# Performance work log

Measured on AMD Instinct MI355X. Metric: run time of the kernel, lower is better.

The kernel has to match this reference:

```python
import jax, jax.numpy as jnp
import numpy as np

B, C, IMG, P, G = 512, 3, 128, 16, 8
DIM, HEADS, DH, DEPTH, MLP, NCLS, K = 384, 6, 64, 12, 1536, 1000, 16
N = G * G + 1  # 65 tokens (cls + 8x8 patches)
INNER = HEADS * DH
PD = C * P * P  # patch_dim = 768


def _rel_pos_index(g):
    coords = np.stack(np.meshgrid(np.arange(g), np.arange(g), indexing='ij')).reshape(2, -1)
    rel = (coords[:, :, None] - coords[:, None, :]).transpose(1, 2, 0)
    rel[..., 0] += g - 1
    rel[..., 1] += g - 1
    rel[..., 0] *= 2 * g - 1
    return jnp.asarray(rel.sum(-1))  # [g*g, g*g] int

REL_IDX = _rel_pos_index(G)


def _ln(x, w, b, eps=1e-5):
    mu = jnp.mean(x, -1, keepdims=True)
    var = jnp.mean((x - mu) ** 2, -1, keepdims=True)
    return (x - mu) * jax.lax.rsqrt(var + eps) * w + b


def setup_inputs() -> dict:
    key = jax.random.key(0)
    ks = iter(jax.random.split(key, 48))
    nrm = lambda shape, s=0.02: jax.random.normal(next(ks), shape, jnp.float32) * s
    return {
        'img': jax.random.normal(next(ks), (B, C, IMG, IMG), jnp.float32),
        'pe_ln1_w': jnp.ones((PD,), jnp.float32), 'pe_ln1_b': jnp.zeros((PD,), jnp.float32),
        'pe_w': nrm((PD, DIM)), 'pe_b': jnp.zeros((DIM,), jnp.float32),
        'pe_ln2_w': jnp.ones((DIM,), jnp.float32), 'pe_ln2_b': jnp.zeros((DIM,), jnp.float32),
        'cls_token': nrm((1, DIM), 1.0), 'pos_emb': nrm((N, DIM), 1.0),
        'attn_ln_w': jnp.ones((DEPTH, DIM), jnp.float32), 'attn_ln_b': jnp.zeros((DEPTH, DIM), jnp.float32),
        'qkv_w': nrm((DEPTH, DIM, 3 * INNER)),
        'out_w': nrm((DEPTH, INNER, DIM)), 'out_b': jnp.zeros((DEPTH, DIM), jnp.float32),
        'bias_tables': nrm((DEPTH, (2 * G - 1) * (2 * G - 1))),
        'ff_ln_w': jnp.ones((DEPTH, DIM), jnp.float32), 'ff_ln_b': jnp.zeros((DEPTH, DIM), jnp.float32),
        'ff_w1': nrm((DEPTH, DIM, MLP)), 'ff_b1': jnp.zeros((DEPTH, MLP), jnp.float32),
        'ff_w2': nrm((DEPTH, MLP, DIM)), 'ff_b2': jnp.zeros((DEPTH, DIM), jnp.float32),
        'final_ln_w': jnp.ones((DIM,), jnp.float32), 'final_ln_b': jnp.zeros((DIM,), jnp.float32),
        'head_w': nrm((DIM, NCLS)), 'head_b': jnp.zeros((NCLS,), jnp.float32),
    }


def reference(img, pe_ln1_w, pe_ln1_b, pe_w, pe_b, pe_ln2_w, pe_ln2_b, cls_token, pos_emb,
              attn_ln_w, attn_ln_b, qkv_w, out_w, out_b, bias_tables,
              ff_ln_w, ff_ln_b, ff_w1, ff_b1, ff_w2, ff_b2,
              final_ln_w, final_ln_b, head_w, head_b):
    b = img.shape[0]
    gh = IMG // P
    # b c (h p1) (w p2) -> b (h w) (p1 p2 c)
    x = img.reshape(b, C, gh, P, gh, P).transpose(0, 2, 4, 3, 5, 1).reshape(b, gh * gh, P * P * C)
    x = _ln(x, pe_ln1_w, pe_ln1_b)
    x = _ln(x @ pe_w + pe_b, pe_ln2_w, pe_ln2_b)
    cls = jnp.broadcast_to(cls_token[None], (b, 1, DIM))
    x = jnp.concatenate([cls, x], axis=1) + pos_emb[:N]
    scale = DH ** -0.5
    neg = jnp.finfo(jnp.float32).min  # == -finfo.max, matching torch masked_fill
    for i in range(DEPTH):
        h = _ln(x, attn_ln_w[i], attn_ln_b[i])
        qkv = h @ qkv_w[i]  # [b, N, 3*INNER]
        q, k, v = jnp.split(qkv, 3, axis=-1)
        q, k, v = [t.reshape(b, N, HEADS, DH).transpose(0, 2, 1, 3) for t in (q, k, v)]
        dots = jnp.einsum('bhid,bhjd->bhij', q, k) * scale
        full_bias = jnp.zeros((N, N), jnp.float32).at[1:, 1:].set(bias_tables[i][REL_IDX])
        dots = dots + full_bias
        _, idx = jax.lax.top_k(dots, K)  # per-query top-k keys
        mask = jnp.put_along_axis(jnp.zeros(dots.shape, bool), idx, True, axis=-1, inplace=False)
        attn = jax.nn.softmax(jnp.where(mask, dots, neg), axis=-1)
        o = jnp.einsum('bhij,bhjd->bhid', attn, v).transpose(0, 2, 1, 3).reshape(b, N, INNER)
        x = o @ out_w[i] + out_b[i] + x
        h = _ln(x, ff_ln_w[i], ff_ln_b[i])
        h = jax.nn.gelu(h @ ff_w1[i] + ff_b1[i], approximate=False)
        x = h @ ff_w2[i] + ff_b2[i] + x
    x = _ln(x, final_ln_w, final_ln_b)
    return x[:, 0] @ head_w + head_b
```

## Files before the change

### kernel.cpp

```cpp
#include <hip/hip_runtime.h>
#include <cstdint>
#include <cstddef>


typedef __attribute__((ext_vector_type(8))) short bf16x8;
typedef __attribute__((ext_vector_type(4))) float f32x4;
typedef __attribute__((ext_vector_type(4))) unsigned short u16x4;

__device__ __forceinline__ unsigned short f2bf(float f) {
  unsigned u = __float_as_uint(f);
  u += 0x7FFF + ((u >> 16) & 1);
  return (unsigned short)(u >> 16);
}
__device__ __forceinline__ float bf2f(unsigned short h) {
  return __uint_as_float(((unsigned)h) << 16);
}
__device__ __forceinline__ float gelu_f(float v) {
  return 0.5f * v * (1.f + erff(v * 0.70710678118654752440f));
}

typedef const __attribute__((address_space(1))) unsigned int* gas1_t;
typedef __attribute__((address_space(3))) unsigned int* las3_t;
__device__ __forceinline__ void async16(const void* g, void* l) {
  __builtin_amdgcn_global_load_lds((gas1_t)g, (las3_t)l, 16, 0, 0);
}

__global__ void k_tconv(const float* __restrict__ in, unsigned short* __restrict__ out,
                        int K, int N, int Npad, int total) {
  int idx = blockIdx.x * 256 + threadIdx.x;
  if (idx >= total) return;
  int per = Npad * K;
  int mat = idx / per;
  int rem = idx - mat * per;
  int n = rem / K;
  int kk = rem - n * K;
  float v = 0.f;
  if (n < N) v = in[(size_t)mat * K * N + (size_t)kk * N + n];
  out[idx] = f2bf(v);
}

__global__ void k_padhb(const float* __restrict__ hb, float* __restrict__ out) {
  int i = blockIdx.x * 256 + threadIdx.x;
  if (i < 1024) out[i] = (i < 1000) ? hb[i] : 0.f;
}

__global__ void k_patchln(const float* __restrict__ img,
                          const float* __restrict__ w1, const float* __restrict__ b1,
                          unsigned short* __restrict__ Xp) {
  const int p = blockIdx.x;
  const int b = p >> 6, pl = p & 63;
  const int gr = pl >> 3, gc = pl & 7;
  const int t = threadIdx.x;
  __shared__ float buf[768];
  __shared__ float ps[4], ps2[4];
#pragma unroll
  for (int s = 0; s < 3; ++s) {
    int rr = s * 16 + (t >> 4);
    int c = rr >> 4, p1 = rr & 15, p2 = t & 15;
    float v = img[(((size_t)b * 3 + c) * 128 + (gr * 16 + p1)) * 128 + gc * 16 + p2];
    buf[(p1 * 16 + p2) * 3 + c] = v;
  }
  __syncthreads();
  float e0 = buf[t], e1 = buf[t + 256], e2 = buf[t + 512];
  float s = e0 + e1 + e2;
  float s2 = e0 * e0 + e1 * e1 + e2 * e2;
  for (int off = 32; off; off >>= 1) { s += __shfl_xor(s, off); s2 += __shfl_xor(s2, off); }
  if ((t & 63) == 0) { ps[t >> 6] = s; ps2[t >> 6] = s2; }
  __syncthreads();
  float S = ps[0] + ps[1] + ps[2] + ps[3];
  float S2 = ps2[0] + ps2[1] + ps2[2] + ps2[3];
  float mu = S * (1.f / 768.f);
  float rs = rsqrtf(S2 * (1.f / 768.f) - mu * mu + 1e-5f);
  size_t ob = (size_t)p * 768;
  Xp[ob + t]       = f2bf((e0 - mu) * rs * w1[t]       + b1[t]);
  Xp[ob + t + 256] = f2bf((e1 - mu) * rs * w1[t + 256] + b1[t + 256]);
  Xp[ob + t + 512] = f2bf((e2 - mu) * rs * w1[t + 512] + b1[t + 512]);
}

__global__ void k_ln384(const float* __restrict__ X, const float* __restrict__ w,
                        const float* __restrict__ bb, unsigned short* __restrict__ H) {
  const int row = blockIdx.x;
  const int t = threadIdx.x;
  const float* xr = X + (size_t)row * 384;
  float e0 = xr[t], e1 = xr[t + 128], e2 = xr[t + 256];
  float s = e0 + e1 + e2, s2 = e0 * e0 + e1 * e1 + e2 * e2;
  for (int off = 32; off; off >>= 1) { s += __shfl_xor(s, off); s2 += __shfl_xor(s2, off); }
  __shared__ float ps[2], ps2[2];
  if ((t & 63) == 0) { ps[t >> 6] = s; ps2[t >> 6] = s2; }
  __syncthreads();
  float S = ps[0] + ps[1], S2 = ps2[0] + ps2[1];
  float mu = S * (1.f / 384.f);
  float rs = rsqrtf(S2 * (1.f / 384.f) - mu * mu + 1e-5f);
  size_t ob = (size_t)row * 384;
  H[ob + t]       = f2bf((e0 - mu) * rs * w[t]       + bb[t]);
  H[ob + t + 128] = f2bf((e1 - mu) * rs * w[t + 128] + bb[t + 128]);
  H[ob + t + 256] = f2bf((e2 - mu) * rs * w[t + 256] + bb[t + 256]);
}

__global__ void k_lncls(const float* __restrict__ X, const float* __restrict__ w,
                        const float* __restrict__ bb, unsigned short* __restrict__ H) {
  const int b = blockIdx.x;
  const int t = threadIdx.x;
  const float* xr = X + (size_t)b * 65 * 384;
  float e0 = xr[t], e1 = xr[t + 128], e2 = xr[t + 256];
  float s = e0 + e1 + e2, s2 = e0 * e0 + e1 * e1 + e2 * e2;
  for (int off = 32; off; off >>= 1) { s += __shfl_xor(s, off); s2 += __shfl_xor(s2, off); }
  __shared__ float ps[2], ps2[2];
  if ((t & 63) == 0) { ps[t >> 6] = s; ps2[t >> 6] = s2; }
  __syncthreads();
  float S = ps[0] + ps[1], S2 = ps2[0] + ps2[1];
  float mu = S * (1.f / 384.f);
  float rs = rsqrtf(S2 * (1.f / 384.f) - mu * mu + 1e-5f);
  size_t ob = (size_t)b * 384;
  H[ob + t]       = f2bf((e0 - mu) * rs * w[t]       + bb[t]);
  H[ob + t + 128] = f2bf((e1 - mu) * rs * w[t + 128] + bb[t + 128]);
  H[ob + t + 256] = f2bf((e2 - mu) * rs * w[t + 256] + bb[t + 256]);
}

__global__ void k_ln2pos(const float* __restrict__ tmp, const float* __restrict__ w,
                         const float* __restrict__ bb, const float* __restrict__ pos,
                         float* __restrict__ Xout) {
  const int p = blockIdx.x;
  const int b = p >> 6, pl = p & 63;
  const int t = threadIdx.x;
  const float* xr = tmp + (size_t)p * 384;
  float e0 = xr[t], e1 = xr[t + 128], e2 = xr[t + 256];
  float s = e0 + e1 + e2, s2 = e0 * e0 + e1 * e1 + e2 * e2;
  for (int off = 32; off; off >>= 1) { s += __shfl_xor(s, off); s2 += __shfl_xor(s2, off); }
  __shared__ float ps[2], ps2[2];
  if ((t & 63) == 0) { ps[t >> 6] = s; ps2[t >> 6] = s2; }
  __syncthreads();
  float S = ps[0] + ps[1], S2 = ps2[0] + ps2[1];
  float mu = S * (1.f / 384.f);
  float rs = rsqrtf(S2 * (1.f / 384.f) - mu * mu + 1e-5f);
  const float* pr = pos + (size_t)(1 + pl) * 384;
  float* orow = Xout + ((size_t)b * 65 + 1 + pl) * 384;
  orow[t]       = (e0 - mu) * rs * w[t]       + bb[t]       + pr[t];
  orow[t + 128] = (e1 - mu) * rs * w[t + 128] + bb[t + 128] + pr[t + 128];
  orow[t + 256] = (e2 - mu) * rs * w[t + 256] + bb[t + 256] + pr[t + 256];
}

__global__ void k_cls(const float* __restrict__ cls, const float* __restrict__ pos,
                      float* __restrict__ Xout) {
  int idx = blockIdx.x * 256 + threadIdx.x;
  if (idx >= 512 * 384) return;
  int b = idx / 384, d = idx - b * 384;
  Xout[(size_t)b * 65 * 384 + d] = cls[d] + pos[d];
}

template <int EPI, int OUTBF>
__global__ __launch_bounds__(256, 2) void k_gemm(
    const unsigned short* __restrict__ A,
    const unsigned short* __restrict__ Wt,
    const float* __restrict__ bias,
    const float* __restrict__ Res,
    void* __restrict__ Out,
    int K, int Nreal) {
  __shared__ alignas(16) unsigned short As[128 * 64];
  __shared__ alignas(16) unsigned short Bs[128 * 64];
  const int t = threadIdx.x;
  const int w = t >> 6, l = t & 63;
  const int m0 = blockIdx.x * 128, n0 = blockIdx.y * 128;
  const int wm = w & 1, wn = w >> 1;

  f32x4 acc[4][4] = {};

  const int rA = t >> 3;
  const int cb = t & 7;
  const unsigned short* Ag = A + (size_t)(m0 + rA) * K + cb * 8;
  const unsigned short* Bg = Wt + (size_t)(n0 + rA) * K + cb * 8;

  for (int k0 = 0; k0 < K; k0 += 64) {
#pragma unroll
    for (int p = 0; p < 4; ++p) {
      async16(Ag + (size_t)(p * 32) * K + k0, &As[p * 2048 + t * 8]);
      async16(Bg + (size_t)(p * 32) * K + k0, &Bs[p * 2048 + t * 8]);
    }
    __syncthreads();
#pragma unroll
    for (int kk = 0; kk < 64; kk += 32) {
      bf16x8 af[4], bfr[4];
      const int kof = kk + (l >> 4) * 8;
      const int rsel = l & 15;
#pragma unroll
      for (int i = 0; i < 4; ++i) {
        af[i]  = *(const bf16x8*)&As[(wm * 64 + i * 16 + rsel) * 64 + kof];
        bfr[i] = *(const bf16x8*)&Bs[(wn * 64 + i * 16 + rsel) * 64 + kof];
      }
#pragma unroll
      for (int i = 0; i < 4; ++i)
#pragma unroll
        for (int j = 0; j < 4; ++j)
          acc[i][j] = __builtin_amdgcn_mfma_f32_16x16x32_bf16(af[i], bfr[j], acc[i][j], 0, 0, 0);
    }
    __syncthreads();
  }

  const int colq = l & 15, rowq = (l >> 4) * 4;
#pragma unroll
  for (int i = 0; i < 4; ++i) {
    const int rb = m0 + wm * 64 + i * 16 + rowq;
#pragma unroll
    for (int j = 0; j < 4; ++j) {
      const int c = n0 + wn * 64 + j * 16 + colq;
      float bv = 0.f;
      if (EPI >= 1) bv = bias[c];
#pragma unroll
      for (int rg = 0; rg < 4; ++rg) {
        const int r = rb + rg;
        float v = acc[i][j][rg] + bv;
        if (EPI == 2) v = gelu_f(v);
        if (EPI == 3) v += Res[(size_t)r * Nreal + c];
        if (c < Nreal) {
          if (OUTBF) ((unsigned short*)Out)[(size_t)r * Nreal + c] = f2bf(v);
          else       ((float*)Out)[(size_t)r * Nreal + c] = v;
        }
      }
    }
  }
}

__global__ __launch_bounds__(256, 3) void k_attn(
    const unsigned short* __restrict__ qkvb,
    const float* __restrict__ btab,
    unsigned short* __restrict__ Obuf) {
  const int blk = blockIdx.x;
  const int b = blk / 6, h = blk - b * 6;
  __shared__ alignas(16) union UU {
    unsigned short qk[2 * 80 * 64];
    float ds[65 * 66];
  } u;
  __shared__ alignas(16) float vs[65 * 64];
  __shared__ float wsel[65 * 16];
  __shared__ int   seli[65 * 16];
  const int t = threadIdx.x;
  const size_t base = (size_t)b * 65 * 1152 + h * 64;

  for (int idx = t; idx < 520; idx += 256) {
    int r = idx >> 3, c = idx & 7;
    async16(qkvb + base + (size_t)r * 1152 + c * 8, &u.qk[idx * 8]);
  }
  for (int idx = t; idx < 520; idx += 256) {
    int r = idx >> 3, c = idx & 7;
    async16(qkvb + base + (size_t)r * 1152 + 384 + c * 8, &u.qk[80 * 64 + idx * 8]);
  }
  for (int idx = t; idx < 520; idx += 256) {
    int r = idx >> 3, c = idx & 7;
    bf16x8 raw = *(const bf16x8*)(qkvb + base + (size_t)r * 1152 + 768 + c * 8);
    float* dst = &vs[r * 64 + c * 8];
    f32x4 lo = {bf2f((unsigned short)raw[0]), bf2f((unsigned short)raw[1]),
                bf2f((unsigned short)raw[2]), bf2f((unsigned short)raw[3])};
    f32x4 hi = {bf2f((unsigned short)raw[4]), bf2f((unsigned short)raw[5]),
                bf2f((unsigned short)raw[6]), bf2f((unsigned short)raw[7])};
    *(f32x4*)dst = lo;
    *(f32x4*)(dst + 4) = hi;
  }
  __syncthreads();

  const int w = t >> 6, l = t & 63;
  f32x4 accs[7];
#pragma unroll
  for (int s = 0; s < 7; ++s) {
    int tt = w + s * 4;
    f32x4 a = {0.f, 0.f, 0.f, 0.f};
    if (tt < 25) {
      int it = tt / 5, jt = tt - it * 5;
#pragma unroll
      for (int kk = 0; kk < 64; kk += 32) {
        int kof = kk + (l >> 4) * 8;
        bf16x8 qa = *(const bf16x8*)&u.qk[(it * 16 + (l & 15)) * 64 + kof];
        bf16x8 kb = *(const bf16x8*)&u.qk[80 * 64 + (jt * 16 + (l & 15)) * 64 + kof];
        a = __builtin_amdgcn_mfma_f32_16x16x32_bf16(qa, kb, a, 0, 0, 0);
      }
    }
    accs[s] = a;
  }
  __syncthreads();

#pragma unroll
  for (int s = 0; s < 7; ++s) {
    int tt = w + s * 4;
    if (tt < 25) {
      int it = tt / 5, jt = tt - it * 5;
      int j = jt * 16 + (l & 15);
      int ib = it * 16 + (l >> 4) * 4;
      if (j < 65) {
#pragma unroll
        for (int rg = 0; rg < 4; ++rg) {
          int i = ib + rg;
          if (i < 65) {
            float bias = 0.f;
            if (i > 0 && j > 0) {
              int ri = (i - 1) >> 3, ci = (i - 1) & 7;
              int rj = (j - 1) >> 3, cj = (j - 1) & 7;
              bias = btab[(ri - rj + 7) * 15 + (ci - cj + 7)];
            }
            u.ds[i * 66 + j] = accs[s][rg] * 0.125f + bias;
          }
        }
      }
    }
  }
  __syncthreads();

  if (t < 65) {
    const float* dr = &u.ds[t * 66];
    float lva[16];
    int lia[16];
#pragma unroll
    for (int i = 0; i < 16; ++i) { lva[i] = -3.4e38f; lia[i] = 0; }
    for (int j = 0; j < 65; ++j) {
      float v = dr[j];
      bool c[16];
#pragma unroll
      for (int i = 0; i < 16; ++i) c[i] = v > lva[i];
#pragma unroll
      for (int i = 15; i >= 1; --i) {
        lva[i] = c[i] ? (c[i - 1] ? lva[i - 1] : v) : lva[i];
        lia[i] = c[i] ? (c[i - 1] ? lia[i - 1] : j) : lia[i];
      }
      lva[0] = c[0] ? v : lva[0];
      lia[0] = c[0] ? j : lia[0];
    }
    float m0 = lva[0];
    float sum = 0.f;
    float wsv[16];
#pragma unroll
    for (int i = 0; i < 16; ++i) { wsv[i] = __expf(lva[i] - m0); sum += wsv[i]; }
    float inv = 1.f / sum;
#pragma unroll
    for (int i = 0; i < 16; ++i) {
      wsel[t * 16 + i] = wsv[i] * inv;
      seli[t * 16 + i] = lia[i];
    }
  }
  __syncthreads();

  const size_t obase = (size_t)b * 65 * 384 + h * 64;
  for (int task = t; task < 65 * 16; task += 256) {
    int i = task >> 4, dc = task & 15;
    f32x4 a = {0.f, 0.f, 0.f, 0.f};
    for (int s = 0; s < 16; ++s) {
      float wv = wsel[i * 16 + s];
      int j = seli[i * 16 + s];
      f32x4 vv = *(const f32x4*)&vs[j * 64 + dc * 4];
      a.x += wv * vv.x; a.y += wv * vv.y; a.z += wv * vv.z; a.w += wv * vv.w;
    }
    u16x4 o = {f2bf(a.x), f2bf(a.y), f2bf(a.z), f2bf(a.w)};
    *(u16x4*)&Obuf[obase + (size_t)i * 384 + dc * 4] = o;
  }
}

extern "C" void kernel_launch(void* const* d_in, const int* in_sizes, int n_in,
                              void* d_out, int out_size, void* d_ws, size_t ws_size,
                              hipStream_t stream) {
  (void)in_sizes; (void)n_in; (void)out_size; (void)ws_size;
  const float* img       = (const float*)d_in[0];
  const float* pe_ln1_w  = (const float*)d_in[1];
  const float* pe_ln1_b  = (const float*)d_in[2];
  const float* pe_w      = (const float*)d_in[3];
  const float* pe_b      = (const float*)d_in[4];
  const float* pe_ln2_w  = (const float*)d_in[5];
  const float* pe_ln2_b  = (const float*)d_in[6];
  const float* cls_tok   = (const float*)d_in[7];
  const float* pos_emb   = (const float*)d_in[8];
  const float* attn_ln_w = (const float*)d_in[9];
  const float* attn_ln_b = (const float*)d_in[10];
  const float* qkv_w     = (const float*)d_in[11];
  const float* out_w     = (const float*)d_in[12];
  const float* out_b     = (const float*)d_in[13];
  const float* btab      = (const float*)d_in[14];
  const float* ff_ln_w   = (const float*)d_in[15];
  const float* ff_ln_b   = (const float*)d_in[16];
  const float* ff_w1     = (const float*)d_in[17];
  const float* ff_b1     = (const float*)d_in[18];
  const float* ff_w2     = (const float*)d_in[19];
  const float* ff_b2     = (const float*)d_in[20];
  const float* fin_ln_w  = (const float*)d_in[21];
  const float* fin_ln_b  = (const float*)d_in[22];
  const float* head_w    = (const float*)d_in[23];
  const float* head_b    = (const float*)d_in[24];

  char* ws = (char*)d_ws;
  unsigned short* wt_pe   = (unsigned short*)(ws + 0);
  unsigned short* wt_qkv  = (unsigned short*)(ws + 589824);
  unsigned short* wt_out  = (unsigned short*)(ws + 11206656);
  unsigned short* wt_ff1  = (unsigned short*)(ws + 14745600);
  unsigned short* wt_ff2  = (unsigned short*)(ws + 28901376);
  unsigned short* wt_head = (unsigned short*)(ws + 43057152);
  float*          hb_pad  = (float*)(ws + 43843584);
  float*          x       = (float*)(ws + 43847680);
  unsigned short* hbuf    = (unsigned short*)(ws + 94965760);
  unsigned short* qkvb    = (unsigned short*)(ws + 120524800);
  unsigned short* h1      = (unsigned short*)(ws + 197201920);
  unsigned short* xcls    = (unsigned short*)(ws + 299438080);

  unsigned short* Xp = qkvb;
  float* tmp = (float*)h1;

  k_tconv<<<dim3((294912 + 255) / 256), 256, 0, stream>>>(pe_w, wt_pe, 768, 384, 384, 294912);
  k_tconv<<<dim3((5308416 + 255) / 256), 256, 0, stream>>>(qkv_w, wt_qkv, 384, 1152, 1152, 5308416);
  k_tconv<<<dim3((1769472 + 255) / 256), 256, 0, stream>>>(out_w, wt_out, 384, 384, 384, 1769472);
  k_tconv<<<dim3((7077888 + 255) / 256), 256, 0, stream>>>(ff_w1, wt_ff1, 384, 1536, 1536, 7077888);
  k_tconv<<<dim3((7077888 + 255) / 256), 256, 0, stream>>>(ff_w2, wt_ff2, 1536, 384, 384, 7077888);
  k_tconv<<<dim3((393216 + 255) / 256), 256, 0, stream>>>(head_w, wt_head, 384, 1000, 1024, 393216);
  k_padhb<<<4, 256, 0, stream>>>(head_b, hb_pad);

  k_patchln<<<32768, 256, 0, stream>>>(img, pe_ln1_w, pe_ln1_b, Xp);
  k_gemm<1, 0><<<dim3(256, 3), 256, 0, stream>>>(Xp, wt_pe, pe_b, nullptr, tmp, 768, 384);
  k_ln2pos<<<32768, 128, 0, stream>>>(tmp, pe_ln2_w, pe_ln2_b, pos_emb, x);
  k_cls<<<768, 256, 0, stream>>>(cls_tok, pos_emb, x);

  for (int lay = 0; lay < 12; ++lay) {
    k_ln384<<<33280, 128, 0, stream>>>(x, attn_ln_w + lay * 384, attn_ln_b + lay * 384, hbuf);
    k_gemm<0, 1><<<dim3(260, 9), 256, 0, stream>>>(hbuf, wt_qkv + (size_t)lay * 442368,
                                                   nullptr, nullptr, qkvb, 384, 1152);
    k_attn<<<3072, 256, 0, stream>>>(qkvb, btab + lay * 225, hbuf);
    k_gemm<3, 0><<<dim3(260, 3), 256, 0, stream>>>(hbuf, wt_out + (size_t)lay * 147456,
                                                   out_b + lay * 384, x, x, 384, 384);
    k_ln384<<<33280, 128, 0, stream>>>(x, ff_ln_w + lay * 384, ff_ln_b + lay * 384, hbuf);
    k_gemm<2, 1><<<dim3(260, 12), 256, 0, stream>>>(hbuf, wt_ff1 + (size_t)lay * 589824,
                                                    ff_b1 + lay * 1536, nullptr, h1, 384, 1536);
    k_gemm<3, 0><<<dim3(260, 3), 256, 0, stream>>>(h1, wt_ff2 + (size_t)lay * 589824,
                                                   ff_b2 + lay * 384, x, x, 1536, 384);
  }

  k_lncls<<<512, 128, 0, stream>>>(x, fin_ln_w, fin_ln_b, xcls);
  k_gemm<1, 0><<<dim3(4, 8), 256, 0, stream>>>(xcls, wt_head, hb_pad, nullptr, d_out, 384, 1000);
}
```

Measured before the change: 5.521 ms.

## Slim attention kernel: bf16 V in LDS, value-only top-k sort network, cached bias table

Keeps V as bf16 in shared memory, loaded with async global-to-LDS copies fused into one loop with Q and K. Stages the bias table in LDS, pads the score rows to stride 67 to avoid bank conflicts, and raises the launch bound to 4 blocks per CU. Top-k now keeps only values in a min/max insertion network, then rescans the row to pick indices by threshold, with a tie-fill pass. This cuts register pressure and LDS use, but tie ordering may differ from the reference and every row is scanned several times.

```diff
diff --git a/kernel.cpp b/kernel.cpp
--- a/kernel.cpp
+++ b/kernel.cpp
@@ -220,7 +220,7 @@
   }
 }
 
-__global__ __launch_bounds__(256, 3) void k_attn(
+__global__ __launch_bounds__(256, 4) void k_attn(
     const unsigned short* __restrict__ qkvb,
     const float* __restrict__ btab,
     unsigned short* __restrict__ Obuf) {
@@ -228,32 +228,22 @@
   const int b = blk / 6, h = blk - b * 6;
   __shared__ alignas(16) union UU {
     unsigned short qk[2 * 80 * 64];
-    float ds[65 * 66];
+    float ds[65 * 67];
   } u;
-  __shared__ alignas(16) float vs[65 * 64];
+  __shared__ alignas(16) unsigned short vsb[65 * 64];
   __shared__ float wsel[65 * 16];
-  __shared__ int   seli[65 * 16];
+  __shared__ short seli[65 * 16];
+  __shared__ float btl[225];
   const int t = threadIdx.x;
   const size_t base = (size_t)b * 65 * 1152 + h * 64;
 
+  if (t < 225) btl[t] = btab[t];
   for (int idx = t; idx < 520; idx += 256) {
     int r = idx >> 3, c = idx & 7;
-    async16(qkvb + base + (size_t)r * 1152 + c * 8, &u.qk[idx * 8]);
-  }
-  for (int idx = t; idx < 520; idx += 256) {
-    int r = idx >> 3, c = idx & 7;
-    async16(qkvb + base + (size_t)r * 1152 + 384 + c * 8, &u.qk[80 * 64 + idx * 8]);
-  }
-  for (int idx = t; idx < 520; idx += 256) {
-    int r = idx >> 3, c = idx & 7;
-    bf16x8 raw = *(const bf16x8*)(qkvb + base + (size_t)r * 1152 + 768 + c * 8);
-    float* dst = &vs[r * 64 + c * 8];
-    f32x4 lo = {bf2f((unsigned short)raw[0]), bf2f((unsigned short)raw[1]),
-                bf2f((unsigned short)raw[2]), bf2f((unsigned short)raw[3])};
-    f32x4 hi = {bf2f((unsigned short)raw[4]), bf2f((unsigned short)raw[5]),
-                bf2f((unsigned short)raw[6]), bf2f((unsigned short)raw[7])};
-    *(f32x4*)dst = lo;
-    *(f32x4*)(dst + 4) = hi;
+    const unsigned short* gp = qkvb + base + (size_t)r * 1152 + c * 8;
+    async16(gp, &u.qk[idx * 8]);
+    async16(gp + 384, &u.qk[80 * 64 + idx * 8]);
+    async16(gp + 768, &vsb[idx * 8]);
   }
   __syncthreads();
 
@@ -293,9 +283,9 @@
             if (i > 0 && j > 0) {
               int ri = (i - 1) >> 3, ci = (i - 1) & 7;
               int rj = (j - 1) >> 3, cj = (j - 1) & 7;
-              bias = btab[(ri - rj + 7) * 15 + (ci - cj + 7)];
+              bias = btl[(ri - rj + 7) * 15 + (ci - cj + 7)];
             }
-            u.ds[i * 66 + j] = accs[s][rg] * 0.125f + bias;
+            u.ds[i * 67 + j] = accs[s][rg] * 0.125f + bias;
           }
         }
       }
@@ -304,49 +294,64 @@
   __syncthreads();
 
   if (t < 65) {
-    const float* dr = &u.ds[t * 66];
-    float lva[16];
-    int lia[16];
-#pragma unroll
-    for (int i = 0; i < 16; ++i) { lva[i] = -3.4e38f; lia[i] = 0; }
+    const float* dr = &u.ds[t * 67];
+    float lv[16];
+#pragma unroll
+    for (int i = 0; i < 16; ++i) lv[i] = -3.4e38f;
+    for (int j = 0; j < 65; ++j) {
+      float x = dr[j];
+#pragma unroll
+      for (int i = 0; i < 16; ++i) {
+        float lo = fminf(lv[i], x);
+        lv[i] = fmaxf(lv[i], x);
+        x = lo;
+      }
+    }
+    float m0 = lv[0];
+    float sum = 0.f;
+#pragma unroll
+    for (int i = 0; i < 16; ++i) sum += __expf(lv[i] - m0);
+    float inv = 1.f / sum;
+    float vt = lv[15];
+    int pos = 0;
     for (int j = 0; j < 65; ++j) {
       float v = dr[j];
-      bool c[16];
-#pragma unroll
-      for (int i = 0; i < 16; ++i) c[i] = v > lva[i];
-#pragma unroll
-      for (int i = 15; i >= 1; --i) {
-        lva[i] = c[i] ? (c[i - 1] ? lva[i - 1] : v) : lva[i];
-        lia[i] = c[i] ? (c[i - 1] ? lia[i - 1] : j) : lia[i];
-      }
-      lva[0] = c[0] ? v : lva[0];
-      lia[0] = c[0] ? j : lia[0];
-    }
-    float m0 = lva[0];
-    float sum = 0.f;
-    float wsv[16];
-#pragma unroll
-    for (int i = 0; i < 16; ++i) { wsv[i] = __expf(lva[i] - m0); sum += wsv[i]; }
-    float inv = 1.f / sum;
-#pragma unroll
-    for (int i = 0; i < 16; ++i) {
-      wsel[t * 16 + i] = wsv[i] * inv;
-      seli[t * 16 + i] = lia[i];
-    }
+      if (v > vt) {
+        wsel[t * 16 + pos] = v;
+        seli[t * 16 + pos] = (short)j;
+        ++pos;
+      }
+    }
+    for (int j = 0; j < 65; ++j) {
+      if (pos >= 16) break;
+      float v = dr[j];
+      if (v == vt) {
+        wsel[t * 16 + pos] = v;
+        seli[t * 16 + pos] = (short)j;
+        ++pos;
+      }
+    }
+#pragma unroll
+    for (int i = 0; i < 16; ++i)
+      wsel[t * 16 + i] = __expf(wsel[t * 16 + i] - m0) * inv;
   }
   __syncthreads();
 
   const size_t obase = (size_t)b * 65 * 384 + h * 64;
   for (int task = t; task < 65 * 16; task += 256) {
     int i = task >> 4, dc = task & 15;
-    f32x4 a = {0.f, 0.f, 0.f, 0.f};
+    float a0 = 0.f, a1 = 0.f, a2 = 0.f, a3 = 0.f;
+#pragma unroll
     for (int s = 0; s < 16; ++s) {
       float wv = wsel[i * 16 + s];
       int j = seli[i * 16 + s];
-      f32x4 vv = *(const f32x4*)&vs[j * 64 + dc * 4];
-      a.x += wv * vv.x; a.y += wv * vv.y; a.z += wv * vv.z; a.w += wv * vv.w;
-    }
-    u16x4 o = {f2bf(a.x), f2bf(a.y), f2bf(a.z), f2bf(a.w)};
+      u16x4 raw = *(const u16x4*)&vsb[j * 64 + dc * 4];
+      a0 += wv * bf2f(raw.x);
+      a1 += wv * bf2f(raw.y);
+      a2 += wv * bf2f(raw.z);
+      a3 += wv * bf2f(raw.w);
+    }
+    u16x4 o = {f2bf(a0), f2bf(a1), f2bf(a2), f2bf(a3)};
     *(u16x4*)&Obuf[obase + (size_t)i * 384 + dc * 4] = o;
   }
 }
```

New measurement: 5.523 ms. Within noise of the previous version (+0.0%).
